# Performance work log

Measured on AMD Instinct MI355X. Metric: run time of the kernel, lower is better.

Reference implementation:

```python
import jax, jax.numpy as jnp
import numpy as np

DIM = 128
N_NODES = 50000
N_EDGES = 625000


def setup_inputs() -> dict:
    key = jax.random.key(0)
    ks = jax.random.split(key, 6)
    X = jax.random.normal(ks[0], (N_NODES, DIM), dtype=jnp.float32)
    edge_index = jax.random.randint(ks[1], (2, N_EDGES), 0, N_NODES, dtype=jnp.int64)
    # Linear params, init like torch (uniform +/- 1/sqrt(dim))
    bound = 1.0 / np.sqrt(DIM)
    msg_w = jax.random.uniform(ks[2], (DIM, DIM), minval=-bound, maxval=bound, dtype=jnp.float32)
    msg_b = jax.random.uniform(ks[3], (DIM,), minval=-bound, maxval=bound, dtype=jnp.float32)
    lin_w = jax.random.uniform(ks[4], (DIM, DIM), minval=-bound, maxval=bound, dtype=jnp.float32)
    lin_b = jax.random.uniform(ks[5], (DIM,), minval=-bound, maxval=bound, dtype=jnp.float32)
    eps = jnp.asarray(0.0, dtype=jnp.float32)
    return {"X": X, "edge_index": edge_index, "eps": eps,
            "msg_w": msg_w, "msg_b": msg_b, "lin_w": lin_w, "lin_b": lin_b}


def reference(X, edge_index, eps, msg_w, msg_b, lin_w, lin_b):
    src, dst = edge_index[0], edge_index[1]
    # msg_lin(X) then gather at dst: (E, F)
    msg = (jnp.einsum('nf,gf->ng', X, msg_w) + msg_b)[dst]
    # scatter-add messages onto src nodes: (N, F)
    agg = jax.ops.segment_sum(msg, src, num_segments=X.shape[0])
    out = (1.0 + eps) * X + agg
    out = jnp.einsum('nf,gf->ng', out, lin_w) + lin_b
    return jax.nn.relu(out)
```

## Files before the change

kernel.cpp:

```cpp
#include <hip/hip_runtime.h>
#include <hip/hip_bf16.h>

#define NN 50000
#define NE 625000
#define DIM 128

#define NBKT 782
#define NBKTP 784
#define CAP 1536
#define CHUNK 4096
#define NCHUNK ((NE + CHUNK - 1) / CHUNK)

#define XCAST_NB 6250
#define PREP_NB 65
#define A_NB (XCAST_NB + PREP_NB + 1)

using fragAB = __attribute__((ext_vector_type(8))) short;
using fragC  = __attribute__((ext_vector_type(4))) float;

__device__ __forceinline__ unsigned short f2bf(float f) {
    unsigned int u = __float_as_uint(f);
    unsigned int r = u + 0x7FFFu + ((u >> 16) & 1u);
    return (unsigned short)(r >> 16);
}

__device__ __forceinline__ float bflo(unsigned v) { return __uint_as_float(v << 16); }
__device__ __forceinline__ float bfhi(unsigned v) { return __uint_as_float(v & 0xffff0000u); }

__global__ __launch_bounds__(256) void prep_cast_kernel(
    const float* __restrict__ X, const float* __restrict__ L,
    const float* __restrict__ W, const float* __restrict__ mb,
    float* __restrict__ cb, unsigned short* __restrict__ Bh,
    unsigned short* __restrict__ Xbf, int* __restrict__ bucket_cursor) {
    int blk = blockIdx.x;
    int t = threadIdx.x;

    if (blk < XCAST_NB) {
        int idx = (blk * 256 + t) * 4;
        float4 v = *(const float4*)(X + idx);
        uint2 p;
        p.x = (unsigned)f2bf(v.x) | ((unsigned)f2bf(v.y) << 16);
        p.y = (unsigned)f2bf(v.z) | ((unsigned)f2bf(v.w) << 16);
        *(uint2*)(Xbf + idx) = p;
        return;
    }
    if (blk < XCAST_NB + PREP_NB) {
        int idx = (blk - XCAST_NB) * 256 + t;
        if (idx < DIM * DIM) {
            int o = idx >> 7, g = idx & 127;
            float s = 0.f;
            for (int f = 0; f < DIM; f++) s += L[o * DIM + f] * W[f * DIM + g];
            Bh[o * 256 + 128 + g] = f2bf(s);
            Bh[o * 256 + g] = f2bf(L[o * DIM + g]);
        } else if (idx < DIM * DIM + DIM) {
            int o = idx - DIM * DIM;
            float s = 0.f;
            for (int f = 0; f < DIM; f++) s += L[o * DIM + f] * mb[f];
            cb[o] = s;
        }
        return;
    }
    for (int i = t; i < NBKTP; i += 256) bucket_cursor[i] = 0;
}

__global__ __launch_bounds__(256) void bin_kernel(const int* __restrict__ ei,
                                                  int* __restrict__ bucket_cursor,
                                                  unsigned* __restrict__ staging) {
    __shared__ int cnt[NBKTP];
    __shared__ int base[NBKTP];
    __shared__ int gb[NBKTP];
    __shared__ int sarr[256];
    __shared__ unsigned staged[CHUNK];
    int t = threadIdx.x;
    int e0 = blockIdx.x * CHUNK;
    int nthis = NE - e0; if (nthis > CHUNK) nthis = CHUNK;

    for (int i = t; i < NBKTP; i += 256) cnt[i] = 0;
    __syncthreads();

    unsigned pk[CHUNK / 256];
#pragma unroll
    for (int i = 0; i < CHUNK / 256; i++) {
        int e = e0 + i * 256 + t;
        if (e < NE) {
            int s = ei[e];
            int d = ei[NE + e];
            unsigned b = (unsigned)s >> 6;
            pk[i] = (b << 22) | ((unsigned)(s & 63) << 16) | (unsigned)d;
            atomicAdd(&cnt[b], 1);
        } else pk[i] = 0xFFFFFFFFu;
    }
    __syncthreads();

    int myb = t * 4;
    int s0 = 0;
    if (myb < NBKTP) s0 = cnt[myb] + cnt[myb + 1] + cnt[myb + 2] + cnt[myb + 3];
    sarr[t] = s0;
    __syncthreads();
    for (int off = 1; off < 256; off <<= 1) {
        int v = (t >= off) ? sarr[t - off] : 0;
        __syncthreads();
        sarr[t] += v;
        __syncthreads();
    }
    int run = sarr[t] - s0;
    if (myb < NBKTP) {
        for (int i = 0; i < 4; i++) {
            int b = myb + i;
            base[b] = run;
            int c = cnt[b];
            gb[b] = (b < NBKT && c > 0) ? atomicAdd(&bucket_cursor[b], c) : 0;
            run += c;
        }
    }
    __syncthreads();
    if (myb < NBKTP) {
        for (int i = 0; i < 4; i++) cnt[myb + i] = base[myb + i];
    }
    __syncthreads();

#pragma unroll
    for (int i = 0; i < CHUNK / 256; i++) {
        if (pk[i] != 0xFFFFFFFFu) {
            unsigned b = pk[i] >> 22;
            int pos = atomicAdd(&cnt[b], 1);
            staged[pos] = pk[i];
        }
    }
    __syncthreads();

    for (int idx = t; idx < nthis; idx += 256) {
        unsigned p = staged[idx];
        unsigned b = p >> 22;
        int pos = gb[b] + (idx - base[b]);
        if (pos >= 0 && pos < CAP) staging[(size_t)b * CAP + pos] = p;
    }
}

__global__ __launch_bounds__(512) void bucket_gather(
    const int* __restrict__ bucket_cursor, const unsigned* __restrict__ staging,
    const unsigned short* __restrict__ Xbf, unsigned short* __restrict__ Aggbf,
    int* __restrict__ deg) {
    __shared__ unsigned rec[CAP];
    __shared__ unsigned sorted_[CAP];
    __shared__ int hcnt[64];
    __shared__ int hbase[64];
    __shared__ int cur[64];
    int t = threadIdx.x;
    int b = blockIdx.x;
    int cnt_b = bucket_cursor[b];
    if (cnt_b > CAP) cnt_b = CAP;

    if (t < 64) hcnt[t] = 0;
    __syncthreads();
    for (int i = t; i < cnt_b; i += 512) {
        unsigned r = staging[(size_t)b * CAP + i];
        rec[i] = r;
        atomicAdd(&hcnt[(r >> 16) & 63], 1);
    }
    __syncthreads();
    if (t == 0) {
        int run = 0;
        for (int i = 0; i < 64; i++) { hbase[i] = run; run += hcnt[i]; }
    }
    __syncthreads();
    if (t < 64) {
        cur[t] = hbase[t];
        int src = b * 64 + t;
        if (src < NN) deg[src] = hcnt[t];
    }
    __syncthreads();
    for (int i = t; i < cnt_b; i += 512) {
        unsigned r = rec[i];
        int pos = atomicAdd(&cur[(r >> 16) & 63], 1);
        sorted_[pos] = r;
    }
    __syncthreads();

    int wave = t >> 6, lane = t & 63;
    int l32 = lane & 31, half = lane >> 5;
    const uint2* __restrict__ X2 = (const uint2*)Xbf;
    for (int ni = 0; ni < 8; ni++) {
        int local = wave * 8 + ni;
        int node = b * 64 + local;
        if (node >= NN) continue;
        int start = hbase[local];
        int cnt = hcnt[local];
        float a0 = 0.f, a1 = 0.f, a2 = 0.f, a3 = 0.f;
        int pairs = cnt >> 1;
        int j = 0;
        for (; j + 8 <= pairs; j += 8) {
            int d[8];
#pragma unroll
            for (int i = 0; i < 8; i++)
                d[i] = (int)(sorted_[start + 2 * (j + i) + half] & 0xFFFFu);
            uint2 v[8];
#pragma unroll
            for (int i = 0; i < 8; i++) v[i] = X2[(size_t)d[i] * 32 + l32];
#pragma unroll
            for (int i = 0; i < 8; i++) {
                a0 += bflo(v[i].x);
                a1 += bfhi(v[i].x);
                a2 += bflo(v[i].y);
                a3 += bfhi(v[i].y);
            }
        }
        for (; j < pairs; j++) {
            int d = (int)(sorted_[start + 2 * j + half] & 0xFFFFu);
            uint2 v = X2[(size_t)d * 32 + l32];
            a0 += bflo(v.x);
            a1 += bfhi(v.x);
            a2 += bflo(v.y);
            a3 += bfhi(v.y);
        }
        if ((cnt & 1) && half == 0) {
            int d = (int)(sorted_[start + cnt - 1] & 0xFFFFu);
            uint2 v = X2[(size_t)d * 32 + l32];
            a0 += bflo(v.x);
            a1 += bfhi(v.x);
            a2 += bflo(v.y);
            a3 += bfhi(v.y);
        }
        a0 += __shfl_xor(a0, 32);
        a1 += __shfl_xor(a1, 32);
        a2 += __shfl_xor(a2, 32);
        a3 += __shfl_xor(a3, 32);
        if (half == 0) {
            uint2 p;
            p.x = (unsigned)f2bf(a0) | ((unsigned)f2bf(a1) << 16);
            p.y = (unsigned)f2bf(a2) | ((unsigned)f2bf(a3) << 16);
            ((uint2*)Aggbf)[(size_t)node * 32 + l32] = p;
        }
    }
}

__global__ __launch_bounds__(256) void outgemm_kernel(
    const unsigned short* __restrict__ Xbf, const unsigned short* __restrict__ Aggbf,
    const unsigned short* __restrict__ Bh, const int* __restrict__ deg,
    const float* __restrict__ cb, const float* __restrict__ lin_b,
    const float* __restrict__ epsp, float* __restrict__ out) {
    __shared__ unsigned short As[128 * 40];
    __shared__ unsigned short Bs[128 * 40];
    int tid = threadIdx.x;
    int lane = tid & 63;
    int wave = tid >> 6;
    int m16 = lane & 15;
    int quad = lane >> 4;
    int waveM = (wave & 1) * 64;
    int waveN = (wave >> 1) * 64;
    int r0 = blockIdx.x * 128;
    float scale = 1.0f + *epsp;

    fragC acc[4][4];
#pragma unroll
    for (int i = 0; i < 4; i++)
#pragma unroll
        for (int j = 0; j < 4; j++) acc[i][j] = (fragC){0.f, 0.f, 0.f, 0.f};

    int srow = tid >> 1;
    int shalf = tid & 1;
    int arow = r0 + srow;
    if (arow >= NN) arow = NN - 1;

    for (int kc = 0; kc < 8; kc++) {
        int kb = kc * 32;
        {
            const unsigned short* asrc = (kc < 4) ? Xbf : Aggbf;
            int akb = kb & 127;
            const uint4* gp = (const uint4*)(asrc + (size_t)arow * 128 + akb + shalf * 16);
            uint4 w0 = gp[0];
            uint4 w1 = gp[1];
            uint4* lp = (uint4*)(As + srow * 40 + shalf * 16);
            lp[0] = w0;
            lp[1] = w1;
        }
        {
            const uint4* gp = (const uint4*)(Bh + (size_t)srow * 256 + kb + shalf * 16);
            uint4 w0 = gp[0];
            uint4 w1 = gp[1];
            if (kb < 128) {
                unsigned int* u0 = (unsigned int*)&w0;
                unsigned int* u1 = (unsigned int*)&w1;
#pragma unroll
                for (int q = 0; q < 4; q++) {
                    float lo = bflo(u0[q]) * scale;
                    float hi = bfhi(u0[q]) * scale;
                    u0[q] = (unsigned)f2bf(lo) | ((unsigned)f2bf(hi) << 16);
                    lo = bflo(u1[q]) * scale;
                    hi = bfhi(u1[q]) * scale;
                    u1[q] = (unsigned)f2bf(lo) | ((unsigned)f2bf(hi) << 16);
                }
            }
            uint4* lp = (uint4*)(Bs + srow * 40 + shalf * 16);
            lp[0] = w0;
            lp[1] = w1;
        }
        __syncthreads();

        fragAB a[4], bfr[4];
#pragma unroll
        for (int i = 0; i < 4; i++)
            a[i] = *(const fragAB*)(As + (waveM + i * 16 + m16) * 40 + quad * 8);
#pragma unroll
        for (int j = 0; j < 4; j++)
            bfr[j] = *(const fragAB*)(Bs + (waveN + j * 16 + m16) * 40 + quad * 8);
#pragma unroll
        for (int i = 0; i < 4; i++)
#pragma unroll
            for (int j = 0; j < 4; j++)
                acc[i][j] = __builtin_amdgcn_mfma_f32_16x16x32_bf16(a[i], bfr[j], acc[i][j], 0, 0, 0);
        __syncthreads();
    }

#pragma unroll
    for (int j = 0; j < 4; j++) {
        int col = waveN + j * 16 + m16;
        float cbc = cb[col];
        float lbc = lin_b[col];
#pragma unroll
        for (int i = 0; i < 4; i++) {
            int rbase = r0 + waveM + i * 16 + quad * 4;
#pragma unroll
            for (int r = 0; r < 4; r++) {
                int row = rbase + r;
                if (row < NN) {
                    float dg = (float)deg[row];
                    float v = acc[i][j][r] + dg * cbc + lbc;
                    out[(size_t)row * 128 + col] = fmaxf(v, 0.f);
                }
            }
        }
    }
}

extern "C" void kernel_launch(void* const* d_in, const int* in_sizes, int n_in,
                              void* d_out, int out_size, void* d_ws, size_t ws_size,
                              hipStream_t stream) {
    const float* X = (const float*)d_in[0];
    const int* ei = (const int*)d_in[1];
    const float* epsp = (const float*)d_in[2];
    const float* msg_w = (const float*)d_in[3];
    const float* msg_b = (const float*)d_in[4];
    const float* lin_w = (const float*)d_in[5];
    const float* lin_b = (const float*)d_in[6];
    float* out = (float*)d_out;

    int* bucket_cursor = (int*)d_ws;
    unsigned* staging = (unsigned*)(bucket_cursor + 800);
    int* deg = (int*)(staging + (size_t)NBKT * CAP);
    float* cb = (float*)(deg + NN);
    unsigned short* Bh = (unsigned short*)(cb + DIM);
    unsigned short* Xbf = Bh + 128 * 256;
    unsigned short* Aggbf = Xbf + (size_t)NN * 128;

    prep_cast_kernel<<<A_NB, 256, 0, stream>>>(X, lin_w, msg_w, msg_b, cb, Bh, Xbf,
                                               bucket_cursor);
    bin_kernel<<<NCHUNK, 256, 0, stream>>>(ei, bucket_cursor, staging);
    bucket_gather<<<NBKT, 512, 0, stream>>>(bucket_cursor, staging, Xbf, Aggbf, deg);
    outgemm_kernel<<<(NN + 127) / 128, 256, 0, stream>>>(Xbf, Aggbf, Bh, deg, cb, lin_b,
                                                         epsp, out);
}
```

Before: 166.7 us.

## Merge prep/cast and binning kernels; gather per-wave edge streams across nodes

Folds the X bf16 cast and weight-prep work into the edge-binning kernel as extra blocks, and moves the bucket-cursor zeroing to a memset, so the two setup phases share one launch and can overlap. The gather phase now has each wave walk the contiguous sorted edge range of its 8 nodes as a single stream, with every lane loading one 32-bit slice of the row. Each node's sum is flushed when the node id changes, and nodes with no edges are zeroed explicitly. This removes the per-node pair/half split and the cross-half shuffle reduction, and keeps loads in flight across node boundaries, at the cost of a branchy flush inside the unrolled loop and narrower per-lane loads.

After: 180.7 us. 1.08x slower.

```diff
diff --git a/kernel.cpp b/kernel.cpp
--- a/kernel.cpp
+++ b/kernel.cpp
@@ -13,7 +13,7 @@
 
 #define XCAST_NB 6250
 #define PREP_NB 65
-#define A_NB (XCAST_NB + PREP_NB + 1)
+#define SETUP_NB (NCHUNK + XCAST_NB + PREP_NB)
 
 using fragAB = __attribute__((ext_vector_type(8))) short;
 using fragC  = __attribute__((ext_vector_type(4))) float;
@@ -27,52 +27,48 @@
 __device__ __forceinline__ float bflo(unsigned v) { return __uint_as_float(v << 16); }
 __device__ __forceinline__ float bfhi(unsigned v) { return __uint_as_float(v & 0xffff0000u); }
 
-__global__ __launch_bounds__(256) void prep_cast_kernel(
-    const float* __restrict__ X, const float* __restrict__ L,
-    const float* __restrict__ W, const float* __restrict__ mb,
-    float* __restrict__ cb, unsigned short* __restrict__ Bh,
-    unsigned short* __restrict__ Xbf, int* __restrict__ bucket_cursor) {
-    int blk = blockIdx.x;
-    int t = threadIdx.x;
-
-    if (blk < XCAST_NB) {
-        int idx = (blk * 256 + t) * 4;
-        float4 v = *(const float4*)(X + idx);
-        uint2 p;
-        p.x = (unsigned)f2bf(v.x) | ((unsigned)f2bf(v.y) << 16);
-        p.y = (unsigned)f2bf(v.z) | ((unsigned)f2bf(v.w) << 16);
-        *(uint2*)(Xbf + idx) = p;
-        return;
-    }
-    if (blk < XCAST_NB + PREP_NB) {
-        int idx = (blk - XCAST_NB) * 256 + t;
-        if (idx < DIM * DIM) {
-            int o = idx >> 7, g = idx & 127;
-            float s = 0.f;
-            for (int f = 0; f < DIM; f++) s += L[o * DIM + f] * W[f * DIM + g];
-            Bh[o * 256 + 128 + g] = f2bf(s);
-            Bh[o * 256 + g] = f2bf(L[o * DIM + g]);
-        } else if (idx < DIM * DIM + DIM) {
-            int o = idx - DIM * DIM;
-            float s = 0.f;
-            for (int f = 0; f < DIM; f++) s += L[o * DIM + f] * mb[f];
-            cb[o] = s;
-        }
-        return;
-    }
-    for (int i = t; i < NBKTP; i += 256) bucket_cursor[i] = 0;
-}
-
-__global__ __launch_bounds__(256) void bin_kernel(const int* __restrict__ ei,
-                                                  int* __restrict__ bucket_cursor,
-                                                  unsigned* __restrict__ staging) {
+__global__ __launch_bounds__(256) void mega_setup(
+    const float* __restrict__ X, const int* __restrict__ ei,
+    const float* __restrict__ L, const float* __restrict__ W,
+    const float* __restrict__ mb, float* __restrict__ cb,
+    unsigned short* __restrict__ Bh, unsigned short* __restrict__ Xbf,
+    int* __restrict__ bucket_cursor, unsigned* __restrict__ staging) {
     __shared__ int cnt[NBKTP];
     __shared__ int base[NBKTP];
     __shared__ int gb[NBKTP];
     __shared__ int sarr[256];
     __shared__ unsigned staged[CHUNK];
+    int blk = blockIdx.x;
     int t = threadIdx.x;
-    int e0 = blockIdx.x * CHUNK;
+
+    if (blk >= NCHUNK) {
+        int xb = blk - NCHUNK;
+        if (xb < XCAST_NB) {
+            int idx = (xb * 256 + t) * 4;
+            float4 v = *(const float4*)(X + idx);
+            uint2 p;
+            p.x = (unsigned)f2bf(v.x) | ((unsigned)f2bf(v.y) << 16);
+            p.y = (unsigned)f2bf(v.z) | ((unsigned)f2bf(v.w) << 16);
+            *(uint2*)(Xbf + idx) = p;
+        } else {
+            int idx = (xb - XCAST_NB) * 256 + t;
+            if (idx < DIM * DIM) {
+                int o = idx >> 7, g = idx & 127;
+                float s = 0.f;
+                for (int f = 0; f < DIM; f++) s += L[o * DIM + f] * W[f * DIM + g];
+                Bh[o * 256 + 128 + g] = f2bf(s);
+                Bh[o * 256 + g] = f2bf(L[o * DIM + g]);
+            } else if (idx < DIM * DIM + DIM) {
+                int o = idx - DIM * DIM;
+                float s = 0.f;
+                for (int f = 0; f < DIM; f++) s += L[o * DIM + f] * mb[f];
+                cb[o] = s;
+            }
+        }
+        return;
+    }
+
+    int e0 = blk * CHUNK;
     int nthis = NE - e0; if (nthis > CHUNK) nthis = CHUNK;
 
     for (int i = t; i < NBKTP; i += 256) cnt[i] = 0;
@@ -177,60 +173,48 @@
     }
     __syncthreads();
 
-    int wave = t >> 6, lane = t & 63;
-    int l32 = lane & 31, half = lane >> 5;
-    const uint2* __restrict__ X2 = (const uint2*)Xbf;
+    int w = t >> 6, lane = t & 63;
+    const unsigned* __restrict__ Xd = (const unsigned*)Xbf;
+    unsigned* __restrict__ Ao = (unsigned*)Aggbf;
+    int gs = hbase[w * 8];
+    int ge = (w < 7) ? hbase[w * 8 + 8] : cnt_b;
+    int cur_nl = -1;
+    float ax = 0.f, ay = 0.f;
+    for (int base2 = gs; base2 < ge; base2 += 8) {
+        int nb = ge - base2; if (nb > 8) nb = 8;
+        unsigned r[8];
+        unsigned v[8];
+#pragma unroll
+        for (int i = 0; i < 8; i++) r[i] = (i < nb) ? sorted_[base2 + i] : 0u;
+#pragma unroll
+        for (int i = 0; i < 8; i++)
+            if (i < nb) v[i] = Xd[(size_t)(r[i] & 0xFFFFu) * 64 + lane];
+#pragma unroll
+        for (int i = 0; i < 8; i++) {
+            if (i < nb) {
+                int nl = (r[i] >> 16) & 63;
+                if (nl != cur_nl) {
+                    if (cur_nl >= 0) {
+                        unsigned pk = (unsigned)f2bf(ax) | ((unsigned)f2bf(ay) << 16);
+                        Ao[(size_t)(b * 64 + cur_nl) * 64 + lane] = pk;
+                    }
+                    cur_nl = nl;
+                    ax = 0.f; ay = 0.f;
+                }
+                ax += bflo(v[i]);
+                ay += bfhi(v[i]);
+            }
+        }
+    }
+    if (cur_nl >= 0) {
+        unsigned pk = (unsigned)f2bf(ax) | ((unsigned)f2bf(ay) << 16);
+        Ao[(size_t)(b * 64 + cur_nl) * 64 + lane] = pk;
+    }
+#pragma unroll
     for (int ni = 0; ni < 8; ni++) {
-        int local = wave * 8 + ni;
+        int local = w * 8 + ni;
         int node = b * 64 + local;
-        if (node >= NN) continue;
-        int start = hbase[local];
-        int cnt = hcnt[local];
-        float a0 = 0.f, a1 = 0.f, a2 = 0.f, a3 = 0.f;
-        int pairs = cnt >> 1;
-        int j = 0;
-        for (; j + 8 <= pairs; j += 8) {
-            int d[8];
-#pragma unroll
-            for (int i = 0; i < 8; i++)
-                d[i] = (int)(sorted_[start + 2 * (j + i) + half] & 0xFFFFu);
-            uint2 v[8];
-#pragma unroll
-            for (int i = 0; i < 8; i++) v[i] = X2[(size_t)d[i] * 32 + l32];
-#pragma unroll
-            for (int i = 0; i < 8; i++) {
-                a0 += bflo(v[i].x);
-                a1 += bfhi(v[i].x);
-                a2 += bflo(v[i].y);
-                a3 += bfhi(v[i].y);
-            }
-        }
-        for (; j < pairs; j++) {
-            int d = (int)(sorted_[start + 2 * j + half] & 0xFFFFu);
-            uint2 v = X2[(size_t)d * 32 + l32];
-            a0 += bflo(v.x);
-            a1 += bfhi(v.x);
-            a2 += bflo(v.y);
-            a3 += bfhi(v.y);
-        }
-        if ((cnt & 1) && half == 0) {
-            int d = (int)(sorted_[start + cnt - 1] & 0xFFFFu);
-            uint2 v = X2[(size_t)d * 32 + l32];
-            a0 += bflo(v.x);
-            a1 += bfhi(v.x);
-            a2 += bflo(v.y);
-            a3 += bfhi(v.y);
-        }
-        a0 += __shfl_xor(a0, 32);
-        a1 += __shfl_xor(a1, 32);
-        a2 += __shfl_xor(a2, 32);
-        a3 += __shfl_xor(a3, 32);
-        if (half == 0) {
-            uint2 p;
-            p.x = (unsigned)f2bf(a0) | ((unsigned)f2bf(a1) << 16);
-            p.y = (unsigned)f2bf(a2) | ((unsigned)f2bf(a3) << 16);
-            ((uint2*)Aggbf)[(size_t)node * 32 + l32] = p;
-        }
+        if (node < NN && hcnt[local] == 0) Ao[(size_t)node * 64 + lane] = 0u;
     }
 }
 
@@ -353,9 +337,10 @@
     unsigned short* Xbf = Bh + 128 * 256;
     unsigned short* Aggbf = Xbf + (size_t)NN * 128;
 
-    prep_cast_kernel<<<A_NB, 256, 0, stream>>>(X, lin_w, msg_w, msg_b, cb, Bh, Xbf,
-                                               bucket_cursor);
-    bin_kernel<<<NCHUNK, 256, 0, stream>>>(ei, bucket_cursor, staging);
+    hipMemsetAsync(bucket_cursor, 0, NBKTP * sizeof(int), stream);
+
+    mega_setup<<<SETUP_NB, 256, 0, stream>>>(X, ei, lin_w, msg_w, msg_b, cb, Bh, Xbf,
+                                             bucket_cursor, staging);
     bucket_gather<<<NBKT, 512, 0, stream>>>(bucket_cursor, staging, Xbf, Aggbf, deg);
     outgemm_kernel<<<(NN + 127) / 128, 256, 0, stream>>>(Xbf, Aggbf, Bh, deg, cb, lin_b,
                                                          epsp, out);
```
